# Optimization experiments

Hardware: AMD Instinct MI355X
Metric: run time of the kernel (lower is better)

The kernel has to match this reference:

```python
import jax, jax.numpy as jnp
import numpy as np

HEADS = 4
SCALE = 10.0
DIM = 128
VOL = (16, 16, 16)
BATCH = 2
EPS = 1e-12  # F.normalize eps


def setup_inputs() -> dict:
    key = jax.random.key(0)
    ks = jax.random.split(key, 7)
    h, w, z = VOL
    shape = (BATCH, DIM, h, w, z)
    wstd = 1.0 / np.sqrt(DIM)
    return {
        "x": jax.random.normal(ks[0], shape, dtype=jnp.float32),
        "cond_x": jax.random.normal(ks[1], shape, dtype=jnp.float32),
        "Wq": jax.random.normal(ks[2], (DIM, DIM), dtype=jnp.float32) * wstd,
        "bq": jnp.zeros((DIM,), dtype=jnp.float32),
        "Wk": jax.random.normal(ks[3], (DIM, DIM), dtype=jnp.float32) * wstd,
        "bk": jnp.zeros((DIM,), dtype=jnp.float32),
        "Wv": jax.random.normal(ks[4], (DIM, DIM), dtype=jnp.float32) * wstd,
        "bv": jnp.zeros((DIM,), dtype=jnp.float32),
        "Wo": jax.random.normal(ks[5], (DIM, DIM), dtype=jnp.float32) * wstd,
        "bo": jnp.zeros((DIM,), dtype=jnp.float32),
    }


def _l2norm_last(t):
    # F.normalize(t, dim=-1): divide by max(||t||_2, eps) along last axis
    n = jnp.sqrt(jnp.sum(t * t, axis=-1, keepdims=True))
    return t / jnp.maximum(n, EPS)


def reference(x, cond_x, Wq, bq, Wk, bk, Wv, bv, Wo, bo):
    b, c, h, w, z = x.shape
    N = h * w * z
    d = c // HEADS
    xf = x.reshape(b, c, N)          # conv1x1 == per-voxel linear over channels
    cf = cond_x.reshape(b, c, N)
    q = jnp.einsum('oc,bcn->bon', Wq, xf) + bq[None, :, None]
    k = jnp.einsum('oc,bcn->bon', Wk, cf) + bk[None, :, None]
    v = jnp.einsum('oc,bcn->bon', Wv, cf) + bv[None, :, None]
    # 'b (h c) n -> b h c n'
    q = q.reshape(b, HEADS, d, N)
    k = k.reshape(b, HEADS, d, N)
    v = v.reshape(b, HEADS, d, N)
    # NOTE: original normalizes dim=-1 of [b,h,d,N] -> over the SPATIAL axis
    q = _l2norm_last(q)
    k = _l2norm_last(k)
    sim = jnp.einsum('bhdi,bhdj->bhij', q, k) * SCALE   # [b,h,N,N]
    attn = jax.nn.softmax(sim, axis=-1)
    out = jnp.einsum('bhij,bhdj->bhid', attn, v)        # [b,h,N,d]
    # 'b h n d -> b (h d) n' then back to volume
    out = out.transpose(0, 1, 3, 2).reshape(b, c, N)
    out = jnp.einsum('oc,bcn->bon', Wo, out) + bo[None, :, None]
    return out.reshape(b, c, h, w, z)
```

## Files before the change

### kernel.cpp

```cpp
#include <hip/hip_runtime.h>
#include <hip/hip_bf16.h>
#include <math.h>

#define NSP 4096
#define CD 128
#define NB 2
#define NH 4
#define JS 4
#define JSTEP 64
#define NSTEP ((NSP / JS) / JSTEP)

typedef __attribute__((ext_vector_type(8))) short bf16x8;
typedef __attribute__((ext_vector_type(4))) float f32x4;

static constexpr float QSCALE = 10.0f * 1.4426950408889634f;

__device__ __forceinline__ ushort f2bf(float f) {
    union { float f; unsigned u; } v; v.f = f;
    unsigned r = v.u + 0x7fffu + ((v.u >> 16) & 1u);
    return (ushort)(r >> 16);
}
__device__ __forceinline__ float bf2f(ushort u) {
    union { unsigned u; float f; } v; v.u = ((unsigned)u) << 16;
    return v.f;
}
__device__ __forceinline__ unsigned pk2bf(float a, float b) {
    union { __hip_bfloat162 h; unsigned u; } t;
    t.h = __float22bfloat162_rn(make_float2(a, b));
    return t.u;
}
__device__ __forceinline__ void gload_lds16(const void* g, void* l) {
    __builtin_amdgcn_global_load_lds(
        (const __attribute__((address_space(1))) unsigned int*)g,
        (__attribute__((address_space(3))) unsigned int*)l, 16, 0, 0);
}

__global__ __launch_bounds__(256) void cast_all(
    const float* __restrict__ x, const float* __restrict__ cx,
    const float* __restrict__ Wq, const float* __restrict__ Wk,
    const float* __restrict__ Wv, const float* __restrict__ Wo,
    ushort* __restrict__ Xt, ushort* __restrict__ Ct, ushort* __restrict__ Wall)
{
    const int t = threadIdx.x;
    if (blockIdx.x >= 128) {
        const int sub = blockIdx.x - 128;
        const int m = blockIdx.z * 2 + blockIdx.y;
        const float* src = (m == 0) ? Wq : (m == 1) ? Wk : (m == 2) ? Wv : Wo;
        const int off = sub * 1024 + t * 4;
        const float4 v = *(const float4*)(src + off);
        ushort4 o;
        o.x = f2bf(v.x); o.y = f2bf(v.y); o.z = f2bf(v.z); o.w = f2bf(v.w);
        *(ushort4*)(Wall + m * 16384 + off) = o;
        return;
    }
    __shared__ ushort L[32][130];
    const int n0 = blockIdx.x * 32;
    const int b  = blockIdx.y;
    const float* in = (blockIdx.z == 0) ? x : cx;
    ushort* outp    = (blockIdx.z == 0) ? Xt : Ct;
    const int nl = t & 31, cq = t >> 5;
    #pragma unroll
    for (int cc = cq; cc < CD; cc += 8)
        L[nl][cc] = f2bf(in[((size_t)b * CD + cc) * NSP + n0 + nl]);
    __syncthreads();
    const int nr = t >> 3, cs = (t & 7) * 16;
    unsigned u[8];
    #pragma unroll
    for (int w = 0; w < 8; ++w)
        u[w] = (unsigned)L[nr][cs + 2 * w] | ((unsigned)L[nr][cs + 2 * w + 1] << 16);
    ushort* dst = outp + ((size_t)(b * NSP + n0 + nr)) * CD + cs;
    *(uint4*)(dst)     = make_uint4(u[0], u[1], u[2], u[3]);
    *(uint4*)(dst + 8) = make_uint4(u[4], u[5], u[6], u[7]);
}

__global__ __launch_bounds__(256) void proj_qkv_mfma(
    const ushort* __restrict__ Xt, const ushort* __restrict__ Ct,
    const ushort* __restrict__ Wall,
    const float* __restrict__ Bq, const float* __restrict__ Bk, const float* __restrict__ Bv,
    ushort* __restrict__ Qt, ushort* __restrict__ Kt, ushort* __restrict__ V16,
    float* __restrict__ partQ, float* __restrict__ partK)
{
    const int t = threadIdx.x;
    const int wid = t >> 6, lane = t & 63;
    const int g = lane >> 4, n16 = lane & 15;
    const int nt = blockIdx.x;
    const int b  = nt >> 8;
    const int xblk = nt & 255;
    const int nb = xblk * 16;
    const int o0 = (blockIdx.y * 4 + wid) * 16;

    const ushort* Wq = Wall;
    const ushort* Wk = Wall + 16384;
    const ushort* Wv = Wall + 32768;
    const size_t xrow = ((size_t)(b * NSP + nb + n16)) * CD;
    const size_t wrow = (size_t)(o0 + n16) * CD;

    f32x4 aq = {0,0,0,0}, ak = {0,0,0,0}, av = {0,0,0,0};
    #pragma unroll
    for (int ks = 0; ks < 4; ++ks) {
        const int k0 = ks * 32 + g * 8;
        const bf16x8 bx = *(const bf16x8*)(Xt + xrow + k0);
        const bf16x8 bc = *(const bf16x8*)(Ct + xrow + k0);
        const bf16x8 wqf = *(const bf16x8*)(Wq + wrow + k0);
        const bf16x8 wkf = *(const bf16x8*)(Wk + wrow + k0);
        const bf16x8 wvf = *(const bf16x8*)(Wv + wrow + k0);
        aq = __builtin_amdgcn_mfma_f32_16x16x32_bf16(wqf, bx, aq, 0, 0, 0);
        ak = __builtin_amdgcn_mfma_f32_16x16x32_bf16(wkf, bc, ak, 0, 0, 0);
        av = __builtin_amdgcn_mfma_f32_16x16x32_bf16(wvf, bc, av, 0, 0, 0);
    }
    const int jb = nb >> 6, jr = (nb & 63) + n16;
    float sq[4], sk[4];
    #pragma unroll
    for (int r = 0; r < 4; ++r) {
        const int o = o0 + 4 * g + r;
        const float qv = aq[r] + Bq[o];
        const float kv = ak[r] + Bk[o];
        V16[((size_t)(b * CD + o)) * NSP + nb + n16] = f2bf(av[r] + Bv[o]);
        const int bh = b * NH + (o >> 5);
        const size_t idx = (((size_t)(bh * 64 + jb)) * 4 + ((o & 31) >> 3)) * 512
                         + jr * 8 + (o & 7);
        Qt[idx] = f2bf(qv);
        Kt[idx] = f2bf(kv);
        sq[r] = qv * qv; sk[r] = kv * kv;
    }
    #pragma unroll
    for (int r = 0; r < 4; ++r) {
        #pragma unroll
        for (int off = 1; off < 16; off <<= 1) {
            sq[r] += __shfl_xor(sq[r], off);
            sk[r] += __shfl_xor(sk[r], off);
        }
    }
    if (n16 == 0) {
        #pragma unroll
        for (int r = 0; r < 4; ++r) {
            const int ch = b * CD + o0 + 4 * g + r;
            partQ[(size_t)ch * 256 + xblk] = sq[r];
            partK[(size_t)ch * 256 + xblk] = sk[r];
        }
    }
}

__global__ __launch_bounds__(256) void normfin(
    const float* __restrict__ partQ, const float* __restrict__ partK,
    float* __restrict__ fsc)
{
    const int ch = blockIdx.x;
    const int t = threadIdx.x;
    float vq = partQ[(size_t)ch * 256 + t];
    float vk = partK[(size_t)ch * 256 + t];
    #pragma unroll
    for (int off = 32; off > 0; off >>= 1) {
        vq += __shfl_down(vq, off, 64);
        vk += __shfl_down(vk, off, 64);
    }
    __shared__ float redq[4], redk[4];
    if ((t & 63) == 0) { redq[t >> 6] = vq; redk[t >> 6] = vk; }
    __syncthreads();
    if (t == 0) {
        const float nq = sqrtf(redq[0] + redq[1] + redq[2] + redq[3]);
        const float nk = sqrtf(redk[0] + redk[1] + redk[2] + redk[3]);
        fsc[ch] = QSCALE / (fmaxf(nq, 1e-12f) * fmaxf(nk, 1e-12f));
    }
}

__global__ __launch_bounds__(256, 4) void attn_mfma(
    const ushort* __restrict__ Qt, const ushort* __restrict__ Kt,
    const ushort* __restrict__ V16, const float* __restrict__ fsc,
    unsigned* __restrict__ pacc, float* __restrict__ pl)
{
    __shared__ __align__(16) ushort Kl[4][2048];
    __shared__ __align__(16) ushort Vl[4][2048];

    const int t = threadIdx.x;
    const int wid = t >> 6, lane = t & 63;
    const int g = lane >> 4, n16 = lane & 15;
    const int f = blockIdx.x;
    const int bh = f & 7, it32 = (f >> 3) & 31, js = f >> 8;
    const int b = bh >> 2, h = bh & 3;
    const int i0 = it32 * 128 + wid * 32;

    const ushort* QtB = Qt + (size_t)bh * NSP * 32;
    const ushort* KtB = Kt + (size_t)bh * NSP * 32;
    const ushort* Vb  = V16 + (size_t)(b * CD + h * 32) * NSP;

    const float* fb = fsc + b * CD + h * 32 + g * 8;
    const f32x4 fA = *(const f32x4*)(fb);
    const f32x4 fB = *(const f32x4*)(fb + 4);

    const size_t qoff = ((size_t)(i0 >> 6) * 4 + g) * 512 + (size_t)(i0 & 63) * 8;
    const bf16x8 qr0 = *(const bf16x8*)(QtB + qoff + n16 * 8);
    const bf16x8 qr1 = *(const bf16x8*)(QtB + qoff + (16 + n16) * 8);
    auto scaleq = [&](bf16x8 q) -> bf16x8 {
        union { unsigned u[4]; bf16x8 v; } o;
        o.u[0] = pk2bf(bf2f((ushort)q[0]) * fA.x, bf2f((ushort)q[1]) * fA.y);
        o.u[1] = pk2bf(bf2f((ushort)q[2]) * fA.z, bf2f((ushort)q[3]) * fA.w);
        o.u[2] = pk2bf(bf2f((ushort)q[4]) * fB.x, bf2f((ushort)q[5]) * fB.y);
        o.u[3] = pk2bf(bf2f((ushort)q[6]) * fB.z, bf2f((ushort)q[7]) * fB.w);
        return o.v;
    };
    const bf16x8 qf0 = scaleq(qr0);
    const bf16x8 qf1 = scaleq(qr1);

    f32x4 acc00 = {0,0,0,0}, acc01 = {0,0,0,0}, acc10 = {0,0,0,0}, acc11 = {0,0,0,0};
    float l0 = 0.f, l1 = 0.f;
    const f32x4 zero = {0,0,0,0};

    const int klp = lane ^ (wid * 2);
    const int vd  = wid * 8 + (lane >> 3);
    const int vsw = (lane & 7) ^ (lane >> 3);
    auto stageK = [&](int buf, int jt) {
        gload_lds16(KtB + ((size_t)(jt >> 6) * 4 + wid) * 512 + klp * 8,
                    &Kl[buf][wid * 512]);
    };
    auto stageV = [&](int buf, int jt) {
        gload_lds16(Vb + (size_t)vd * NSP + jt + vsw * 8, &Vl[buf][wid * 512]);
    };

    const int jbeg = js * (NSP / JS);
    stageK(0, jbeg);          stageV(0, jbeg);
    stageK(1, jbeg + JSTEP);  stageV(1, jbeg + JSTEP);

    for (int step = 0; step < NSTEP; ++step) {
        const int jt = jbeg + step * JSTEP;
        if (step + 2 < NSTEP) {
            stageK((step + 2) & 3, jt + 2 * JSTEP);
            stageV((step + 2) & 3, jt + 2 * JSTEP);
            asm volatile("s_waitcnt vmcnt(4)" ::: "memory");
        } else if (step + 1 < NSTEP) {
            asm volatile("s_waitcnt vmcnt(2)" ::: "memory");
        } else {
            asm volatile("s_waitcnt vmcnt(0)" ::: "memory");
        }
        __builtin_amdgcn_s_barrier();
        const int cur = step & 3;
        __builtin_amdgcn_s_setprio(1);

        #pragma unroll
        for (int s = 0; s < 2; ++s) {
            const bf16x8 kf0 = *(const bf16x8*)(&Kl[cur][g * 512 + ((s * 32 + n16) ^ (g * 2)) * 8]);
            const bf16x8 kf1 = *(const bf16x8*)(&Kl[cur][g * 512 + ((s * 32 + 16 + n16) ^ (g * 2)) * 8]);
            const int c0 = ((4 * s + (g >> 1)) ^ (n16 & 7)) * 8 + (g & 1) * 4;
            const int c1 = ((4 * s + 2 + (g >> 1)) ^ (n16 & 7)) * 8 + (g & 1) * 4;
            union { uint2 u2[2]; bf16x8 v; } v0, v1;
            v0.u2[0] = *(const uint2*)(&Vl[cur][n16 * 64 + c0]);
            v0.u2[1] = *(const uint2*)(&Vl[cur][n16 * 64 + c1]);
            v1.u2[0] = *(const uint2*)(&Vl[cur][(16 + n16) * 64 + c0]);
            v1.u2[1] = *(const uint2*)(&Vl[cur][(16 + n16) * 64 + c1]);

            #pragma unroll
            for (int it = 0; it < 2; ++it) {
                const bf16x8 qf = it ? qf1 : qf0;
                f32x4 s0 = __builtin_amdgcn_mfma_f32_16x16x32_bf16(kf0, qf, zero, 0, 0, 0);
                f32x4 s1 = __builtin_amdgcn_mfma_f32_16x16x32_bf16(kf1, qf, zero, 0, 0, 0);
                const float p0 = __builtin_amdgcn_exp2f(s0.x);
                const float p1 = __builtin_amdgcn_exp2f(s0.y);
                const float p2 = __builtin_amdgcn_exp2f(s0.z);
                const float p3 = __builtin_amdgcn_exp2f(s0.w);
                const float p4 = __builtin_amdgcn_exp2f(s1.x);
                const float p5 = __builtin_amdgcn_exp2f(s1.y);
                const float p6 = __builtin_amdgcn_exp2f(s1.z);
                const float p7 = __builtin_amdgcn_exp2f(s1.w);
                const float ps = ((p0 + p1) + (p2 + p3)) + ((p4 + p5) + (p6 + p7));
                if (it) l1 += ps; else l0 += ps;
                union { unsigned u[4]; bf16x8 v; } pf;
                pf.u[0] = pk2bf(p0, p1);
                pf.u[1] = pk2bf(p2, p3);
                pf.u[2] = pk2bf(p4, p5);
                pf.u[3] = pk2bf(p6, p7);
                if (it) {
                    acc10 = __builtin_amdgcn_mfma_f32_16x16x32_bf16(v0.v, pf.v, acc10, 0, 0, 0);
                    acc11 = __builtin_amdgcn_mfma_f32_16x16x32_bf16(v1.v, pf.v, acc11, 0, 0, 0);
                } else {
                    acc00 = __builtin_amdgcn_mfma_f32_16x16x32_bf16(v0.v, pf.v, acc00, 0, 0, 0);
                    acc01 = __builtin_amdgcn_mfma_f32_16x16x32_bf16(v1.v, pf.v, acc01, 0, 0, 0);
                }
            }
        }
        __builtin_amdgcn_s_setprio(0);
    }

    l0 += __shfl_xor(l0, 16); l0 += __shfl_xor(l0, 32);
    l1 += __shfl_xor(l1, 16); l1 += __shfl_xor(l1, 32);

    const size_t base = (size_t)js * 8 + bh;
    if (lane < 16) {
        pl[base * NSP + i0 + n16]      = l0;
        pl[base * NSP + i0 + 16 + n16] = l1;
    }
    unsigned* pb = pacc + base * 16 * NSP;
    const int col0 = i0 + n16, col1 = i0 + 16 + n16;
    pb[(size_t)(2 * g)     * NSP + col0] = pk2bf(acc00[0], acc00[1]);
    pb[(size_t)(2 * g + 1) * NSP + col0] = pk2bf(acc00[2], acc00[3]);
    pb[(size_t)(8 + 2 * g)     * NSP + col0] = pk2bf(acc01[0], acc01[1]);
    pb[(size_t)(8 + 2 * g + 1) * NSP + col0] = pk2bf(acc01[2], acc01[3]);
    pb[(size_t)(2 * g)     * NSP + col1] = pk2bf(acc10[0], acc10[1]);
    pb[(size_t)(2 * g + 1) * NSP + col1] = pk2bf(acc10[2], acc10[3]);
    pb[(size_t)(8 + 2 * g)     * NSP + col1] = pk2bf(acc11[0], acc11[1]);
    pb[(size_t)(8 + 2 * g + 1) * NSP + col1] = pk2bf(acc11[2], acc11[3]);
}

__global__ __launch_bounds__(256) void combine_proj_out(
    const unsigned* __restrict__ pacc, const float* __restrict__ pl,
    const ushort* __restrict__ Wall, const float* __restrict__ Bo,
    float* __restrict__ outp)
{
    __shared__ __align__(16) ushort Yl[16][128];
    const int t = threadIdx.x;
    const int nt = blockIdx.x;
    const int b  = nt >> 8;
    const int nb = (nt & 255) * 16;

    {
        const int nl = t & 15, hh = (t >> 4) & 3, q = t >> 6;
        const int bh = b * NH + hh;
        const int n = nb + nl;
        float L = 0.f;
        #pragma unroll
        for (int s = 0; s < JS; ++s) L += pl[((size_t)(s * 8 + bh)) * NSP + n];
        const float invL = 1.0f / L;
        unsigned u[4];
        #pragma unroll
        for (int e = 0; e < 4; ++e) {
            const int dp = q * 4 + e;
            float a0 = 0.f, a1 = 0.f;
            #pragma unroll
            for (int s = 0; s < JS; ++s) {
                const unsigned w = pacc[(((size_t)(s * 8 + bh)) * 16 + dp) * NSP + n];
                union { unsigned u; float f; } lo, hi;
                lo.u = w << 16; hi.u = w & 0xffff0000u;
                a0 += lo.f; a1 += hi.f;
            }
            u[e] = pk2bf(a0 * invL, a1 * invL);
        }
        const int chunk = hh * 4 + q;
        *(uint4*)(&Yl[nl][((chunk ^ (nl & 7)) * 8)]) = make_uint4(u[0], u[1], u[2], u[3]);
    }
    __syncthreads();

    const int wid = t >> 6, lane = t & 63;
    const int g = lane >> 4, n16 = lane & 15;
    const ushort* Wo = Wall + 49152;
    #pragma unroll
    for (int half = 0; half < 2; ++half) {
        const int o0 = half * 64 + wid * 16;
        const size_t wrow = (size_t)(o0 + n16) * CD;
        f32x4 a = {0,0,0,0};
        #pragma unroll
        for (int ks = 0; ks < 4; ++ks) {
            const bf16x8 wf = *(const bf16x8*)(Wo + wrow + ks * 32 + g * 8);
            const int chunk = ks * 4 + g;
            const bf16x8 yf = *(const bf16x8*)(&Yl[n16][((chunk ^ (n16 & 7)) * 8)]);
            a = __builtin_amdgcn_mfma_f32_16x16x32_bf16(wf, yf, a, 0, 0, 0);
        }
        #pragma unroll
        for (int r = 0; r < 4; ++r) {
            const int o = o0 + 4 * g + r;
            outp[((size_t)(b * CD + o)) * NSP + nb + n16] = a[r] + Bo[o];
        }
    }
}

extern "C" void kernel_launch(void* const* d_in, const int* in_sizes, int n_in,
                              void* d_out, int out_size, void* d_ws, size_t ws_size,
                              hipStream_t stream)
{
    const float* x  = (const float*)d_in[0];
    const float* cx = (const float*)d_in[1];
    const float* Wq = (const float*)d_in[2];
    const float* bq = (const float*)d_in[3];
    const float* Wk = (const float*)d_in[4];
    const float* bk = (const float*)d_in[5];
    const float* Wv = (const float*)d_in[6];
    const float* bv = (const float*)d_in[7];
    const float* Wo = (const float*)d_in[8];
    const float* bo = (const float*)d_in[9];
    float* out = (float*)d_out;

    char* w = (char*)d_ws;
    float*   fsc  = (float*)w;   w += 4096;
    float*   partQ = (float*)w;  w += (size_t)NB * CD * 256 * 4;
    float*   partK = (float*)w;  w += (size_t)NB * CD * 256 * 4;
    ushort*  Qt   = (ushort*)w;  w += (size_t)NB * NH * NSP * 32 * 2;
    ushort*  Kt   = (ushort*)w;  w += (size_t)NB * NH * NSP * 32 * 2;
    ushort*  V16  = (ushort*)w;  w += (size_t)NB * CD * NSP * 2;
    unsigned* pacc = (unsigned*)w; w += (size_t)JS * 8 * 16 * NSP * 4;
    float*   pl   = (float*)w;   w += (size_t)JS * 8 * NSP * 4;
    ushort*  Xt   = (ushort*)w;  w += (size_t)NB * NSP * CD * 2;
    ushort*  Ct   = (ushort*)w;  w += (size_t)NB * NSP * CD * 2;
    ushort*  Wall = (ushort*)w;

    cast_all<<<dim3(144, NB, 2), 256, 0, stream>>>(x, cx, Wq, Wk, Wv, Wo, Xt, Ct, Wall);
    proj_qkv_mfma<<<dim3(512, 2), 256, 0, stream>>>(Xt, Ct, Wall, bq, bk, bv,
                                                    Qt, Kt, V16, partQ, partK);
    normfin<<<dim3(256), 256, 0, stream>>>(partQ, partK, fsc);
    attn_mfma<<<dim3(1024), 256, 0, stream>>>(Qt, Kt, V16, fsc, pacc, pl);
    combine_proj_out<<<dim3(512), 256, 0, stream>>>(pacc, pl, Wall, bo, out);
}
```

Measured before the change: 63.93 us.

## Double key-split count, shrink LDS ring to two buffers, vectorize Q/K stores

Doubles the number of key-axis splits, so the attention kernel launches twice as many blocks, each covering half as many key tiles. The LDS staging ring goes from four buffers to two, with a second barrier after compute before refilling the just-used buffer, and launch bounds are raised to allow more resident blocks. This aims for more occupancy and parallelism, at the cost of twice the partial-accumulator traffic in the combine stage and less prefetch depth. Separately, the projection kernel now packs four bf16 Q/K values per lane into a single 8-byte store instead of scalar stores.

New measurement: 76.39 us. 19.5% more time.

```diff
diff --git a/kernel.cpp b/kernel.cpp
--- a/kernel.cpp
+++ b/kernel.cpp
@@ -6,7 +6,7 @@
 #define CD 128
 #define NB 2
 #define NH 4
-#define JS 4
+#define JS 8
 #define JSTEP 64
 #define NSTEP ((NSP / JS) / JSTEP)
 
@@ -109,19 +109,26 @@
         av = __builtin_amdgcn_mfma_f32_16x16x32_bf16(wvf, bc, av, 0, 0, 0);
     }
     const int jb = nb >> 6, jr = (nb & 63) + n16;
-    float sq[4], sk[4];
+    float qv[4], kv[4], sq[4], sk[4];
     #pragma unroll
     for (int r = 0; r < 4; ++r) {
         const int o = o0 + 4 * g + r;
-        const float qv = aq[r] + Bq[o];
-        const float kv = ak[r] + Bk[o];
+        qv[r] = aq[r] + Bq[o];
+        kv[r] = ak[r] + Bk[o];
         V16[((size_t)(b * CD + o)) * NSP + nb + n16] = f2bf(av[r] + Bv[o]);
-        const int bh = b * NH + (o >> 5);
-        const size_t idx = (((size_t)(bh * 64 + jb)) * 4 + ((o & 31) >> 3)) * 512
-                         + jr * 8 + (o & 7);
-        Qt[idx] = f2bf(qv);
-        Kt[idx] = f2bf(kv);
-        sq[r] = qv * qv; sk[r] = kv * kv;
+        sq[r] = qv[r] * qv[r]; sk[r] = kv[r] * kv[r];
+    }
+    {
+        const int o_first = o0 + 4 * g;
+        const int bh = b * NH + (o_first >> 5);
+        const int chunk = ((o_first & 31) >> 3);
+        const size_t idx = (((size_t)(bh * 64 + jb)) * 4 + chunk) * 512
+                         + (size_t)jr * 8 + 4 * (g & 1);
+        uint2 qs, ks2;
+        qs.x  = pk2bf(qv[0], qv[1]); qs.y  = pk2bf(qv[2], qv[3]);
+        ks2.x = pk2bf(kv[0], kv[1]); ks2.y = pk2bf(kv[2], kv[3]);
+        *(uint2*)(Qt + idx) = qs;
+        *(uint2*)(Kt + idx) = ks2;
     }
     #pragma unroll
     for (int r = 0; r < 4; ++r) {
@@ -164,13 +171,13 @@
     }
 }
 
-__global__ __launch_bounds__(256, 4) void attn_mfma(
+__global__ __launch_bounds__(256, 6) void attn_mfma(
     const ushort* __restrict__ Qt, const ushort* __restrict__ Kt,
     const ushort* __restrict__ V16, const float* __restrict__ fsc,
     unsigned* __restrict__ pacc, float* __restrict__ pl)
 {
-    __shared__ __align__(16) ushort Kl[4][2048];
-    __shared__ __align__(16) ushort Vl[4][2048];
+    __shared__ __align__(16) ushort Kl[2][2048];
+    __shared__ __align__(16) ushort Vl[2][2048];
 
     const int t = threadIdx.x;
     const int wid = t >> 6, lane = t & 63;
@@ -222,18 +229,13 @@
     stageK(1, jbeg + JSTEP);  stageV(1, jbeg + JSTEP);
 
     for (int step = 0; step < NSTEP; ++step) {
-        const int jt = jbeg + step * JSTEP;
-        if (step + 2 < NSTEP) {
-            stageK((step + 2) & 3, jt + 2 * JSTEP);
-            stageV((step + 2) & 3, jt + 2 * JSTEP);
-            asm volatile("s_waitcnt vmcnt(4)" ::: "memory");
-        } else if (step + 1 < NSTEP) {
+        if (step + 1 < NSTEP) {
             asm volatile("s_waitcnt vmcnt(2)" ::: "memory");
         } else {
             asm volatile("s_waitcnt vmcnt(0)" ::: "memory");
         }
         __builtin_amdgcn_s_barrier();
-        const int cur = step & 3;
+        const int cur = step & 1;
         __builtin_amdgcn_s_setprio(1);
 
         #pragma unroll
@@ -278,6 +280,11 @@
             }
         }
         __builtin_amdgcn_s_setprio(0);
+        __builtin_amdgcn_s_barrier();
+        if (step + 2 < NSTEP) {
+            const int jn = jbeg + (step + 2) * JSTEP;
+            stageK(cur, jn); stageV(cur, jn);
+        }
     }
 
     l0 += __shfl_xor(l0, 16); l0 += __shfl_xor(l0, 32);
@@ -394,6 +401,6 @@
     proj_qkv_mfma<<<dim3(512, 2), 256, 0, stream>>>(Xt, Ct, Wall, bq, bk, bv,
                                                     Qt, Kt, V16, partQ, partK);
     normfin<<<dim3(256), 256, 0, stream>>>(partQ, partK, fsc);
-    attn_mfma<<<dim3(1024), 256, 0, stream>>>(Qt, Kt, V16, fsc, pacc, pl);
+    attn_mfma<<<dim3(2048), 256, 0, stream>>>(Qt, Kt, V16, fsc, pacc, pl);
     combine_proj_out<<<dim3(512), 256, 0, stream>>>(pacc, pl, Wall, bo, out);
 }
```
